# Kernel optimization log

Hardware: AMD Instinct MI355X
Metric: run time of the kernel (lower is better)

Reference implementation:

```python
import jax, jax.numpy as jnp
import numpy as np

# MoE config (matches init_kwargs)
T = 16384   # tokens
H = 1024    # hidden size
I = 1024    # intermediate size per expert
E = 8       # n_experts
TOPK = 2
RENORMALIZE = True


def setup_inputs() -> dict:
    key = jax.random.key(0)
    ks = jax.random.split(key, 6)
    x = jax.random.normal(ks[0], (T, H), dtype=jnp.float32)
    gating_output = jax.random.normal(ks[1], (T, E), dtype=jnp.float32)
    # fp8-quantized weights simulated as their integer-grid values in fp32;
    # dequant = q * per-expert scalar scale (normalize_e4m3fn_to_native_float8 path)
    w1 = jax.random.normal(ks[2], (E, 2 * I, H), dtype=jnp.float32)  # fused [gate; up]
    w2 = jax.random.normal(ks[3], (E, H, I), dtype=jnp.float32)      # down_proj
    w1_scale = jax.random.uniform(ks[4], (E,), dtype=jnp.float32, minval=0.01, maxval=0.05)
    w2_scale = jax.random.uniform(ks[5], (E,), dtype=jnp.float32, minval=0.01, maxval=0.05)
    return {"x": x, "gating_output": gating_output, "w1": w1, "w2": w2,
            "w1_scale": w1_scale, "w2_scale": w2_scale}


def _moe(x, gating_output, w1, w2, w1_scale, w2_scale):
    # softmax scoring -> top-k routing (use_grouped_topk=False)
    probs = jax.nn.softmax(gating_output, axis=-1)              # [T, E]
    topk_w, topk_idx = jax.lax.top_k(probs, TOPK)               # [T, K]
    if RENORMALIZE:
        topk_w = topk_w / jnp.sum(topk_w, axis=-1, keepdims=True)
    out = jnp.zeros_like(x)
    for e in range(E):  # fixed small expert count: grouped-GEMM reference
        w1e = w1[e] * w1_scale[e]                               # dequant [2I, H]
        w2e = w2[e] * w2_scale[e]                               # dequant [H, I]
        gate = x @ w1e[:I].T                                    # [T, I]
        up = x @ w1e[I:].T                                      # [T, I]
        h = jax.nn.silu(gate) * up                              # SwiGLU
        y = h @ w2e.T                                           # [T, H]
        # per-token routing weight for this expert (0 if not routed)
        coef = jnp.sum(jnp.where(topk_idx == e, topk_w, 0.0), axis=-1)  # [T]
        out = out + coef[:, None] * y
    return out


def reference(x, gating_output, w1, w2, w1_scale, w2_scale):
    return _moe(x, gating_output, w1, w2, w1_scale, w2_scale)
```

## Files before the change

### kernel.cpp

```cpp
#include <hip/hip_runtime.h>
#include <hip/hip_bf16.h>

#define T_TOK 16384
#define H_DIM 1024
#define I_DIM 1024
#define E_NUM 8
#define NPAIR (T_TOK * 2)
#define BM 128
#define BK 64
#define MAX_MT (NPAIR / BM + E_NUM)

typedef float v4f __attribute__((ext_vector_type(4)));
typedef float v16f __attribute__((ext_vector_type(16)));
typedef short v8s __attribute__((ext_vector_type(8)));

__device__ __forceinline__ unsigned short f2bf(float f) {
    unsigned int u = __float_as_uint(f);
    unsigned int r = (u + 0x7fffu + ((u >> 16) & 1u)) >> 16;
    return (unsigned short)r;
}
__device__ __forceinline__ float bf2f(unsigned short s) {
    return __uint_as_float(((unsigned int)s) << 16);
}

__device__ __forceinline__ void gl_lds16(const void* g, void* l) {
    __builtin_amdgcn_global_load_lds(
        (const __attribute__((address_space(1))) void*)g,
        (__attribute__((address_space(3))) void*)l, 16, 0, 0);
}

__device__ __forceinline__ int swz(int row, int unit) {
    return row * 64 + ((unit ^ (row & 7)) << 3);
}

__global__ void k_route(const float* __restrict__ gating,
                        int* __restrict__ tokExp, float* __restrict__ tokW,
                        int* __restrict__ counts) {
    int t = blockIdx.x * 256 + threadIdx.x;
    int lane = threadIdx.x & 63;
    float g[E_NUM];
#pragma unroll
    for (int e = 0; e < E_NUM; e++) g[e] = gating[t * E_NUM + e];
    int i0 = 0; float v0 = g[0];
#pragma unroll
    for (int e = 1; e < E_NUM; e++) if (g[e] > v0) { v0 = g[e]; i0 = e; }
    int i1 = -1; float v1 = -1e30f;
#pragma unroll
    for (int e = 0; e < E_NUM; e++) if (e != i0 && g[e] > v1) { v1 = g[e]; i1 = e; }
    float w0 = 1.f / (1.f + __expf(v1 - v0));
    tokExp[2 * t] = i0; tokExp[2 * t + 1] = i1;
    tokW[2 * t] = w0;   tokW[2 * t + 1] = 1.f - w0;
#pragma unroll
    for (int e = 0; e < E_NUM; e++) {
        unsigned long long mA = __ballot(i0 == e);
        unsigned long long mB = __ballot(i1 == e);
        int c = __popcll(mA) + __popcll(mB);
        if (lane == 0 && c) atomicAdd(&counts[e], c);
    }
}

__global__ void k_scan(const int* __restrict__ counts, int* __restrict__ offsets,
                       int* __restrict__ tileOff, int* __restrict__ cursor) {
    if (threadIdx.x == 0 && blockIdx.x == 0) {
        int o = 0, to = 0;
        for (int e = 0; e < E_NUM; e++) {
            offsets[e] = o; tileOff[e] = to; cursor[e] = o;
            o += counts[e];
            to += (counts[e] + BM - 1) / BM;
        }
        offsets[E_NUM] = o; tileOff[E_NUM] = to;
    }
}

__global__ void k_scatter(const int* __restrict__ tokExp, const float* __restrict__ tokW,
                          int* __restrict__ cursor,
                          int* __restrict__ pairTok, float* __restrict__ pairW,
                          int* __restrict__ invMap) {
    int t = blockIdx.x * 256 + threadIdx.x;
    int lane = threadIdx.x & 63;
#pragma unroll
    for (int k = 0; k < 2; k++) {
        int e = tokExp[2 * t + k];
        int pos = 0;
#pragma unroll
        for (int ex = 0; ex < E_NUM; ex++) {
            unsigned long long m = __ballot(e == ex);
            if (m) {
                int leader = __builtin_ctzll(m);
                int base = 0;
                if (lane == leader) base = atomicAdd(&cursor[ex], __popcll(m));
                base = __shfl(base, leader);
                if (e == ex) pos = base + __popcll(m & ((1ull << lane) - 1ull));
            }
        }
        pairTok[pos] = t;
        pairW[pos] = tokW[2 * t + k];
        invMap[2 * t + k] = pos;
    }
}

__global__ void k_cvt_x(const float* __restrict__ src, unsigned short* __restrict__ dst) {
    size_t i4 = ((size_t)blockIdx.x * 256 + threadIdx.x) * 4;
    float4 v = *(const float4*)(src + i4);
    ushort4 o;
    o.x = f2bf(v.x); o.y = f2bf(v.y); o.z = f2bf(v.z); o.w = f2bf(v.w);
    *(ushort4*)(dst + i4) = o;
}

__global__ void k_cvt_w(const float* __restrict__ src, unsigned short* __restrict__ dst,
                        const float* __restrict__ scale, int shift) {
    size_t i4 = ((size_t)blockIdx.x * 256 + threadIdx.x) * 4;
    float s = scale[i4 >> shift];
    float4 v = *(const float4*)(src + i4);
    ushort4 o;
    o.x = f2bf(v.x * s); o.y = f2bf(v.y * s); o.z = f2bf(v.z * s); o.w = f2bf(v.w * s);
    *(ushort4*)(dst + i4) = o;
}

__global__ __launch_bounds__(512, 4)
void k_gemm1(const unsigned short* __restrict__ xbf,
             const unsigned short* __restrict__ w1bf,
             const int* __restrict__ pairTok,
             const int* __restrict__ offsets, const int* __restrict__ tileOff,
             unsigned short* __restrict__ hbuf) {
    __shared__ unsigned short lA[BM * BK];
    __shared__ unsigned short lB[256 * BK];

    int mt = blockIdx.x;
    if (mt >= tileOff[E_NUM]) return;
    int e = 0;
    while (mt >= tileOff[e + 1]) e++;
    int row0 = offsets[e] + (mt - tileOff[e]) * BM;
    int valid = offsets[e + 1] - row0; if (valid > BM) valid = BM;

    int nt = blockIdx.y;
    int tid = threadIdx.x;
    int lane = tid & 63, wave = tid >> 6;
    int role = wave >> 2, quad = wave & 3;
    int wm = quad >> 1, wn = quad & 1;

    int lr = lane >> 3;
    int lcs = ((lane & 7) ^ lr) * 8;

    const unsigned short* wg = w1bf + (size_t)e * 2 * I_DIM * H_DIM + (size_t)(nt * 128) * H_DIM;
    const unsigned short* wu = wg + (size_t)I_DIM * H_DIM;

    int tokRow[2];
#pragma unroll
    for (int j = 0; j < 2; j++) {
        int r = wave * 16 + j * 8 + lr;
        int rc = r < valid ? r : valid - 1;
        tokRow[j] = pairTok[row0 + rc];
    }
    const unsigned short* bRow[4];
#pragma unroll
    for (int j = 0; j < 4; j++) {
        int brow = wave * 32 + j * 8 + lr;
        bRow[j] = (brow < 128) ? (wg + (size_t)brow * H_DIM)
                               : (wu + (size_t)(brow - 128) * H_DIM);
    }

    v16f acc[2][2];
#pragma unroll
    for (int i = 0; i < 2; i++)
#pragma unroll
        for (int j = 0; j < 2; j++) acc[i][j] = (v16f)0.f;

    for (int ko = 0; ko < H_DIM / BK; ko++) {
        int k0 = ko * BK;
        __syncthreads();
#pragma unroll
        for (int j = 0; j < 2; j++)
            gl_lds16(xbf + (size_t)tokRow[j] * H_DIM + k0 + lcs, lA + (wave * 2 + j) * 512);
#pragma unroll
        for (int j = 0; j < 4; j++)
            gl_lds16(bRow[j] + k0 + lcs, lB + (wave * 4 + j) * 512);
        __syncthreads();
#pragma unroll
        for (int kk = 0; kk < BK; kk += 16) {
            int u = (kk >> 3) + (lane >> 5);
            v8s a[2], b[2];
#pragma unroll
            for (int i = 0; i < 2; i++)
                a[i] = *(const v8s*)(lA + swz(wm * 64 + i * 32 + (lane & 31), u));
#pragma unroll
            for (int j = 0; j < 2; j++)
                b[j] = *(const v8s*)(lB + swz(role * 128 + wn * 64 + j * 32 + (lane & 31), u));
#pragma unroll
            for (int i = 0; i < 2; i++)
#pragma unroll
                for (int j = 0; j < 2; j++)
                    acc[i][j] = __builtin_amdgcn_mfma_f32_32x32x16_bf16(a[i], b[j], acc[i][j], 0, 0, 0);
        }
    }

    int half = lane >> 5, c = lane & 31;
    __syncthreads();
    if (role == 1) {
#pragma unroll
        for (int i = 0; i < 2; i++)
#pragma unroll
            for (int r = 0; r < 16; r++) {
                int row = wm * 64 + i * 32 + (r & 3) + 8 * (r >> 2) + 4 * half;
#pragma unroll
                for (int j = 0; j < 2; j++)
                    lB[row * 128 + wn * 64 + j * 32 + c] = f2bf(acc[i][j][r]);
            }
    }
    __syncthreads();
    if (role == 0) {
#pragma unroll
        for (int i = 0; i < 2; i++)
#pragma unroll
            for (int r = 0; r < 16; r++) {
                int row = wm * 64 + i * 32 + (r & 3) + 8 * (r >> 2) + 4 * half;
                if (row < valid) {
                    size_t base = (size_t)(row0 + row) * I_DIM + nt * 128;
#pragma unroll
                    for (int j = 0; j < 2; j++) {
                        float g = acc[i][j][r];
                        float uu = bf2f(lB[row * 128 + wn * 64 + j * 32 + c]);
                        float s = g / (1.f + __expf(-g));
                        hbuf[base + wn * 64 + j * 32 + c] = f2bf(s * uu);
                    }
                }
            }
    }
}

__global__ __launch_bounds__(512, 4)
void k_gemm2(const unsigned short* __restrict__ hbuf,
             const unsigned short* __restrict__ w2bf,
             const float* __restrict__ pairW,
             const int* __restrict__ offsets, const int* __restrict__ tileOff,
             unsigned short* __restrict__ ybuf) {
    __shared__ unsigned short lA[BM * BK];
    __shared__ unsigned short lB[256 * BK];

    int mt = blockIdx.x;
    if (mt >= tileOff[E_NUM]) return;
    int e = 0;
    while (mt >= tileOff[e + 1]) e++;
    int row0 = offsets[e] + (mt - tileOff[e]) * BM;
    int valid = offsets[e + 1] - row0; if (valid > BM) valid = BM;

    int nt = blockIdx.y;
    int tid = threadIdx.x;
    int lane = tid & 63, wave = tid >> 6;
    int wm = wave >> 2, wn = wave & 3;

    int lr = lane >> 3;
    int lcs = ((lane & 7) ^ lr) * 8;

    const unsigned short* w2e = w2bf + (size_t)e * H_DIM * I_DIM + (size_t)(nt * 256) * I_DIM;

    int rowA[2];
#pragma unroll
    for (int j = 0; j < 2; j++) {
        int r = wave * 16 + j * 8 + lr;
        int rc = r < valid ? r : valid - 1;
        rowA[j] = row0 + rc;
    }

    v16f acc[2][2];
#pragma unroll
    for (int i = 0; i < 2; i++)
#pragma unroll
        for (int j = 0; j < 2; j++) acc[i][j] = (v16f)0.f;

    for (int ko = 0; ko < I_DIM / BK; ko++) {
        int k0 = ko * BK;
        __syncthreads();
#pragma unroll
        for (int j = 0; j < 2; j++)
            gl_lds16(hbuf + (size_t)rowA[j] * I_DIM + k0 + lcs, lA + (wave * 2 + j) * 512);
#pragma unroll
        for (int j = 0; j < 4; j++)
            gl_lds16(w2e + (size_t)(wave * 32 + j * 8 + lr) * I_DIM + k0 + lcs,
                     lB + (wave * 4 + j) * 512);
        __syncthreads();
#pragma unroll
        for (int kk = 0; kk < BK; kk += 16) {
            int u = (kk >> 3) + (lane >> 5);
            v8s a[2], b[2];
#pragma unroll
            for (int i = 0; i < 2; i++)
                a[i] = *(const v8s*)(lA + swz(wm * 64 + i * 32 + (lane & 31), u));
#pragma unroll
            for (int j = 0; j < 2; j++)
                b[j] = *(const v8s*)(lB + swz(wn * 64 + j * 32 + (lane & 31), u));
#pragma unroll
            for (int i = 0; i < 2; i++)
#pragma unroll
                for (int j = 0; j < 2; j++)
                    acc[i][j] = __builtin_amdgcn_mfma_f32_32x32x16_bf16(a[i], b[j], acc[i][j], 0, 0, 0);
        }
    }

    int half = lane >> 5, c = lane & 31;
#pragma unroll
    for (int i = 0; i < 2; i++)
#pragma unroll
        for (int r = 0; r < 16; r++) {
            int row = wm * 64 + i * 32 + (r & 3) + 8 * (r >> 2) + 4 * half;
            if (row < valid) {
                int pos = row0 + row;
                float coef = pairW[pos];
                unsigned short* orow = ybuf + (size_t)pos * H_DIM + nt * 256;
#pragma unroll
                for (int j = 0; j < 2; j++)
                    orow[wn * 64 + j * 32 + c] = f2bf(coef * acc[i][j][r]);
            }
        }
}

__global__ __launch_bounds__(256)
void k_reduce(const unsigned short* __restrict__ ybuf,
              const int* __restrict__ invMap,
              float* __restrict__ out) {
    int t = blockIdx.x;
    int p0 = invMap[2 * t], p1 = invMap[2 * t + 1];
    int c4 = threadIdx.x * 4;
    ushort4 a = *(const ushort4*)(ybuf + (size_t)p0 * H_DIM + c4);
    ushort4 b = *(const ushort4*)(ybuf + (size_t)p1 * H_DIM + c4);
    float4 o;
    o.x = bf2f(a.x) + bf2f(b.x);
    o.y = bf2f(a.y) + bf2f(b.y);
    o.z = bf2f(a.z) + bf2f(b.z);
    o.w = bf2f(a.w) + bf2f(b.w);
    *(float4*)(out + (size_t)t * H_DIM + c4) = o;
}

extern "C" void kernel_launch(void* const* d_in, const int* in_sizes, int n_in,
                              void* d_out, int out_size, void* d_ws, size_t ws_size,
                              hipStream_t stream) {
    const float* x      = (const float*)d_in[0];
    const float* gating = (const float*)d_in[1];
    const float* w1     = (const float*)d_in[2];
    const float* w2     = (const float*)d_in[3];
    const float* w1s    = (const float*)d_in[4];
    const float* w2s    = (const float*)d_in[5];
    float* out = (float*)d_out;

    char* ws = (char*)d_ws;
    size_t off = 0;
    auto alloc = [&](size_t bytes) { void* p = ws + off; off += (bytes + 255) & ~(size_t)255; return p; };
    unsigned short* xbf  = (unsigned short*)alloc((size_t)T_TOK * H_DIM * 2);
    unsigned short* w1bf = (unsigned short*)alloc((size_t)E_NUM * 2 * I_DIM * H_DIM * 2);
    unsigned short* w2bf = (unsigned short*)alloc((size_t)E_NUM * H_DIM * I_DIM * 2);
    unsigned short* hbuf = (unsigned short*)alloc((size_t)NPAIR * I_DIM * 2);
    unsigned short* ybuf = (unsigned short*)alloc((size_t)NPAIR * H_DIM * 2);
    int*   pairTok  = (int*)alloc(NPAIR * 4);
    float* pairW    = (float*)alloc(NPAIR * 4);
    int*   tokExp   = (int*)alloc(NPAIR * 4);
    float* tokW     = (float*)alloc(NPAIR * 4);
    int*   invMap   = (int*)alloc(NPAIR * 4);
    int*   counts   = (int*)alloc(64);
    int*   offsets  = (int*)alloc(64);
    int*   tileOff  = (int*)alloc(64);
    int*   cursor   = (int*)alloc(64);

    hipMemsetAsync(counts, 0, 64, stream);

    k_route<<<T_TOK / 256, 256, 0, stream>>>(gating, tokExp, tokW, counts);
    k_scan<<<1, 64, 0, stream>>>(counts, offsets, tileOff, cursor);
    k_scatter<<<T_TOK / 256, 256, 0, stream>>>(tokExp, tokW, cursor, pairTok, pairW, invMap);
    k_cvt_x<<<(T_TOK * H_DIM / 4) / 256, 256, 0, stream>>>(x, xbf);
    k_cvt_w<<<(E_NUM * 2 * I_DIM * H_DIM / 4) / 256, 256, 0, stream>>>(w1, w1bf, w1s, 21);
    k_cvt_w<<<(E_NUM * H_DIM * I_DIM / 4) / 256, 256, 0, stream>>>(w2, w2bf, w2s, 20);

    dim3 g1(MAX_MT, I_DIM / 128);
    k_gemm1<<<g1, 512, 0, stream>>>(xbf, w1bf, pairTok, offsets, tileOff, hbuf);
    dim3 g2(MAX_MT, H_DIM / 256);
    k_gemm2<<<g2, 512, 0, stream>>>(hbuf, w2bf, pairW, offsets, tileOff, ybuf);
    k_reduce<<<T_TOK, 256, 0, stream>>>(ybuf, invMap, out);
}
```

Measured before the change: 561.1 us.

## Use 256x256 tiles with double-buffered LDS and interleaved MFMA/load pipeline

Doubles the M tile to 256 rows so each wave computes a 128x64 sub-tile, which raises arithmetic intensity. Shared memory is double-buffered, and the main loop is split into four phases that interleave LDS reads, async global-to-LDS loads for the stage two iterations ahead, and MFMA bursts under s_setprio and explicit waitcnt. The goal is to hide global load latency and cut the full __syncthreads stalls of the old single-buffer loop. In exchange, occupancy drops to 2 blocks per CU, register pressure is higher, and the larger tiles waste more work on partially filled expert tiles.

Result: slower. 644.7 us (+14.9%).

```diff
diff --git a/kernel.cpp b/kernel.cpp
--- a/kernel.cpp
+++ b/kernel.cpp
@@ -6,8 +6,9 @@
 #define I_DIM 1024
 #define E_NUM 8
 #define NPAIR (T_TOK * 2)
-#define BM 128
+#define BM 256
 #define BK 64
+#define KITER 16
 #define MAX_MT (NPAIR / BM + E_NUM)
 
 typedef float v4f __attribute__((ext_vector_type(4)));
@@ -31,6 +32,37 @@
 
 __device__ __forceinline__ int swz(int row, int unit) {
     return row * 64 + ((unit ^ (row & 7)) << 3);
+}
+
+__device__ __forceinline__ int blkA_of(int w, int j) {
+    int idx = 2 * w + (j & 1);
+    int blk = idx + ((idx >= 8) ? 8 : 0);
+    return blk + ((j >= 2) ? 8 : 0);
+}
+__device__ __forceinline__ int blkB_of(int w, int j) {
+    int idx = 2 * w + (j & 1);
+    int blk = (idx >> 2) * 8 + (idx & 3);
+    return blk + ((j >= 2) ? 4 : 0);
+}
+
+__device__ __forceinline__ void rd_a(const unsigned short* lAc, int rbase, int lane, v8s a[2][4]) {
+#pragma unroll
+    for (int i = 0; i < 2; i++)
+#pragma unroll
+        for (int ks = 0; ks < 4; ks++)
+            a[i][ks] = *(const v8s*)(lAc + swz(rbase + i * 32 + (lane & 31), 2 * ks + (lane >> 5)));
+}
+__device__ __forceinline__ void rd_b(const unsigned short* lBc, int rbase, int lane, v8s b[4]) {
+#pragma unroll
+    for (int ks = 0; ks < 4; ks++)
+        b[ks] = *(const v8s*)(lBc + swz(rbase + (lane & 31), 2 * ks + (lane >> 5)));
+}
+__device__ __forceinline__ void mfma8(const v8s a[2][4], const v8s b[4], v16f* c0, v16f* c1) {
+#pragma unroll
+    for (int ks = 0; ks < 4; ks++) {
+        *c0 = __builtin_amdgcn_mfma_f32_32x32x16_bf16(a[0][ks], b[ks], *c0, 0, 0, 0);
+        *c1 = __builtin_amdgcn_mfma_f32_32x32x16_bf16(a[1][ks], b[ks], *c1, 0, 0, 0);
+    }
 }
 
 __global__ void k_route(const float* __restrict__ gating,
@@ -117,14 +149,65 @@
     *(ushort4*)(dst + i4) = o;
 }
 
-__global__ __launch_bounds__(512, 4)
+#define STG_A(buf, j, k0) gl_lds16(aSrc[j] + (k0) + lcs, &lA[buf][aoff[j]])
+#define STG_B(buf, j, k0) gl_lds16(bSrc[j] + (k0) + lcs, &lB[buf][boff[j]])
+
+#define GEMM_MAINLOOP                                                          \
+    for (int T = 0; T < KITER; T++) {                                          \
+        int cur = T & 1;                                                       \
+        const unsigned short* lAc = lA[cur];                                   \
+        const unsigned short* lBc = lB[cur];                                   \
+        int k2 = (T + 2) * BK;                                                 \
+        bool s2 = (T + 2 < KITER);                                             \
+                                            \
+        rd_a(lAc, wm * 128, lane, a);                                          \
+        rd_b(lBc, bbase, lane, b0);                                            \
+        __builtin_amdgcn_s_barrier();                                          \
+        __builtin_amdgcn_s_setprio(1);                                         \
+        mfma8(a, b0, &acc[0][0], &acc[1][0]);                                  \
+        __builtin_amdgcn_s_setprio(0);                                         \
+        __builtin_amdgcn_s_barrier();                                          \
+                                     \
+        rd_b(lBc, bbase + 32, lane, b1);                                       \
+        if (s2) { STG_B(cur, 0, k2); STG_B(cur, 1, k2); }                      \
+        __builtin_amdgcn_s_barrier();                                          \
+        __builtin_amdgcn_s_setprio(1);                                         \
+        mfma8(a, b1, &acc[0][1], &acc[1][1]);                                  \
+        __builtin_amdgcn_s_setprio(0);                                         \
+        __builtin_amdgcn_s_barrier();                                          \
+                                   \
+        rd_a(lAc, wm * 128 + 64, lane, a);                                     \
+        if (s2) { STG_B(cur, 2, k2); STG_B(cur, 3, k2); }                      \
+        __builtin_amdgcn_s_barrier();                                          \
+        __builtin_amdgcn_s_setprio(1);                                         \
+        mfma8(a, b0, &acc[2][0], &acc[3][0]);                                  \
+        __builtin_amdgcn_s_setprio(0);                                         \
+        __builtin_amdgcn_s_barrier();                                          \
+                          \
+        if (s2) {                                                              \
+            STG_A(cur, 0, k2); STG_A(cur, 1, k2);                              \
+            STG_A(cur, 2, k2); STG_A(cur, 3, k2);                              \
+            asm volatile("s_waitcnt vmcnt(8)" ::: "memory");                    \
+        } else if (T + 1 < KITER) {                                            \
+            asm volatile("s_waitcnt vmcnt(0)" ::: "memory");                    \
+        }                                                                      \
+        __builtin_amdgcn_sched_barrier(0);                                     \
+        __builtin_amdgcn_s_barrier();                                          \
+        __builtin_amdgcn_s_setprio(1);                                         \
+        mfma8(a, b1, &acc[2][1], &acc[3][1]);                                  \
+        __builtin_amdgcn_s_setprio(0);                                         \
+        __builtin_amdgcn_s_barrier();                                          \
+        __builtin_amdgcn_sched_barrier(0);                                     \
+    }
+
+__global__ __launch_bounds__(512, 2)
 void k_gemm1(const unsigned short* __restrict__ xbf,
              const unsigned short* __restrict__ w1bf,
              const int* __restrict__ pairTok,
              const int* __restrict__ offsets, const int* __restrict__ tileOff,
              unsigned short* __restrict__ hbuf) {
-    __shared__ unsigned short lA[BM * BK];
-    __shared__ unsigned short lB[256 * BK];
+    __shared__ unsigned short lA[2][BM * BK];
+    __shared__ unsigned short lB[2][BM * BK];
 
     int mt = blockIdx.x;
     if (mt >= tileOff[E_NUM]) return;
@@ -136,90 +219,75 @@
     int nt = blockIdx.y;
     int tid = threadIdx.x;
     int lane = tid & 63, wave = tid >> 6;
-    int role = wave >> 2, quad = wave & 3;
-    int wm = quad >> 1, wn = quad & 1;
-
+    int wm = wave >> 2, wn = wave & 3;
     int lr = lane >> 3;
     int lcs = ((lane & 7) ^ lr) * 8;
+    int bbase = (wn & 1) * 64 + (wn >> 1) * 128;
 
     const unsigned short* wg = w1bf + (size_t)e * 2 * I_DIM * H_DIM + (size_t)(nt * 128) * H_DIM;
     const unsigned short* wu = wg + (size_t)I_DIM * H_DIM;
 
-    int tokRow[2];
-#pragma unroll
-    for (int j = 0; j < 2; j++) {
-        int r = wave * 16 + j * 8 + lr;
-        int rc = r < valid ? r : valid - 1;
-        tokRow[j] = pairTok[row0 + rc];
-    }
-    const unsigned short* bRow[4];
+    const unsigned short* aSrc[4];
+    const unsigned short* bSrc[4];
+    int aoff[4], boff[4];
 #pragma unroll
     for (int j = 0; j < 4; j++) {
-        int brow = wave * 32 + j * 8 + lr;
-        bRow[j] = (brow < 128) ? (wg + (size_t)brow * H_DIM)
-                               : (wu + (size_t)(brow - 128) * H_DIM);
-    }
-
-    v16f acc[2][2];
-#pragma unroll
-    for (int i = 0; i < 2; i++)
-#pragma unroll
-        for (int j = 0; j < 2; j++) acc[i][j] = (v16f)0.f;
-
-    for (int ko = 0; ko < H_DIM / BK; ko++) {
-        int k0 = ko * BK;
-        __syncthreads();
-#pragma unroll
-        for (int j = 0; j < 2; j++)
-            gl_lds16(xbf + (size_t)tokRow[j] * H_DIM + k0 + lcs, lA + (wave * 2 + j) * 512);
-#pragma unroll
-        for (int j = 0; j < 4; j++)
-            gl_lds16(bRow[j] + k0 + lcs, lB + (wave * 4 + j) * 512);
-        __syncthreads();
-#pragma unroll
-        for (int kk = 0; kk < BK; kk += 16) {
-            int u = (kk >> 3) + (lane >> 5);
-            v8s a[2], b[2];
-#pragma unroll
-            for (int i = 0; i < 2; i++)
-                a[i] = *(const v8s*)(lA + swz(wm * 64 + i * 32 + (lane & 31), u));
-#pragma unroll
-            for (int j = 0; j < 2; j++)
-                b[j] = *(const v8s*)(lB + swz(role * 128 + wn * 64 + j * 32 + (lane & 31), u));
-#pragma unroll
-            for (int i = 0; i < 2; i++)
+        int ab = blkA_of(wave, j), bb = blkB_of(wave, j);
+        aoff[j] = ab * 512; boff[j] = bb * 512;
+        int ra = ab * 8 + lr;
+        int rc = ra < valid ? ra : valid - 1;
+        aSrc[j] = xbf + (size_t)pairTok[row0 + rc] * H_DIM;
+        int rb = bb * 8 + lr;
+        bSrc[j] = (rb < 128) ? (wg + (size_t)rb * H_DIM) : (wu + (size_t)(rb - 128) * H_DIM);
+    }
+
+    v16f acc[4][2];
+#pragma unroll
+    for (int i = 0; i < 4; i++) { acc[i][0] = (v16f)0.f; acc[i][1] = (v16f)0.f; }
+
+#pragma unroll
+    for (int j = 0; j < 4; j++) STG_A(0, j, 0);
+#pragma unroll
+    for (int j = 0; j < 4; j++) STG_B(0, j, 0);
+#pragma unroll
+    for (int j = 0; j < 4; j++) STG_B(1, j, BK);
+#pragma unroll
+    for (int j = 0; j < 4; j++) STG_A(1, j, BK);
+    asm volatile("s_waitcnt vmcnt(8)" ::: "memory");
+    __builtin_amdgcn_sched_barrier(0);
+    __builtin_amdgcn_s_barrier();
+
+    v8s a[2][4], b0[4], b1[4];
+#pragma unroll 2
+    GEMM_MAINLOOP
+
+    __syncthreads();
+    unsigned short* uLds = &lA[0][0];
+    int half = lane >> 5, c = lane & 31;
+    if (wn >= 2) {
+#pragma unroll
+        for (int i = 0; i < 4; i++)
+#pragma unroll
+            for (int r = 0; r < 16; r++) {
+                int row = wm * 128 + i * 32 + (r & 3) + 8 * (r >> 2) + 4 * half;
 #pragma unroll
                 for (int j = 0; j < 2; j++)
-                    acc[i][j] = __builtin_amdgcn_mfma_f32_32x32x16_bf16(a[i], b[j], acc[i][j], 0, 0, 0);
-        }
-    }
-
-    int half = lane >> 5, c = lane & 31;
+                    uLds[row * 128 + (wn - 2) * 64 + j * 32 + c] = f2bf(acc[i][j][r]);
+            }
+    }
     __syncthreads();
-    if (role == 1) {
-#pragma unroll
-        for (int i = 0; i < 2; i++)
+    if (wn < 2) {
+#pragma unroll
+        for (int i = 0; i < 4; i++)
 #pragma unroll
             for (int r = 0; r < 16; r++) {
-                int row = wm * 64 + i * 32 + (r & 3) + 8 * (r >> 2) + 4 * half;
-#pragma unroll
-                for (int j = 0; j < 2; j++)
-                    lB[row * 128 + wn * 64 + j * 32 + c] = f2bf(acc[i][j][r]);
-            }
-    }
-    __syncthreads();
-    if (role == 0) {
-#pragma unroll
-        for (int i = 0; i < 2; i++)
-#pragma unroll
-            for (int r = 0; r < 16; r++) {
-                int row = wm * 64 + i * 32 + (r & 3) + 8 * (r >> 2) + 4 * half;
+                int row = wm * 128 + i * 32 + (r & 3) + 8 * (r >> 2) + 4 * half;
                 if (row < valid) {
                     size_t base = (size_t)(row0 + row) * I_DIM + nt * 128;
 #pragma unroll
                     for (int j = 0; j < 2; j++) {
                         float g = acc[i][j][r];
-                        float uu = bf2f(lB[row * 128 + wn * 64 + j * 32 + c]);
+                        float uu = bf2f(uLds[row * 128 + wn * 64 + j * 32 + c]);
                         float s = g / (1.f + __expf(-g));
                         hbuf[base + wn * 64 + j * 32 + c] = f2bf(s * uu);
                     }
@@ -228,14 +296,14 @@
     }
 }
 
-__global__ __launch_bounds__(512, 4)
+__global__ __launch_bounds__(512, 2)
 void k_gemm2(const unsigned short* __restrict__ hbuf,
              const unsigned short* __restrict__ w2bf,
              const float* __restrict__ pairW,
              const int* __restrict__ offsets, const int* __restrict__ tileOff,
              unsigned short* __restrict__ ybuf) {
-    __shared__ unsigned short lA[BM * BK];
-    __shared__ unsigned short lB[256 * BK];
+    __shared__ unsigned short lA[2][BM * BK];
+    __shared__ unsigned short lB[2][BM * BK];
 
     int mt = blockIdx.x;
     if (mt >= tileOff[E_NUM]) return;
@@ -248,68 +316,58 @@
     int tid = threadIdx.x;
     int lane = tid & 63, wave = tid >> 6;
     int wm = wave >> 2, wn = wave & 3;
-
     int lr = lane >> 3;
     int lcs = ((lane & 7) ^ lr) * 8;
+    int bbase = wn * 64;
 
     const unsigned short* w2e = w2bf + (size_t)e * H_DIM * I_DIM + (size_t)(nt * 256) * I_DIM;
 
-    int rowA[2];
-#pragma unroll
-    for (int j = 0; j < 2; j++) {
-        int r = wave * 16 + j * 8 + lr;
-        int rc = r < valid ? r : valid - 1;
-        rowA[j] = row0 + rc;
-    }
-
-    v16f acc[2][2];
-#pragma unroll
-    for (int i = 0; i < 2; i++)
-#pragma unroll
-        for (int j = 0; j < 2; j++) acc[i][j] = (v16f)0.f;
-
-    for (int ko = 0; ko < I_DIM / BK; ko++) {
-        int k0 = ko * BK;
-        __syncthreads();
-#pragma unroll
-        for (int j = 0; j < 2; j++)
-            gl_lds16(hbuf + (size_t)rowA[j] * I_DIM + k0 + lcs, lA + (wave * 2 + j) * 512);
-#pragma unroll
-        for (int j = 0; j < 4; j++)
-            gl_lds16(w2e + (size_t)(wave * 32 + j * 8 + lr) * I_DIM + k0 + lcs,
-                     lB + (wave * 4 + j) * 512);
-        __syncthreads();
-#pragma unroll
-        for (int kk = 0; kk < BK; kk += 16) {
-            int u = (kk >> 3) + (lane >> 5);
-            v8s a[2], b[2];
-#pragma unroll
-            for (int i = 0; i < 2; i++)
-                a[i] = *(const v8s*)(lA + swz(wm * 64 + i * 32 + (lane & 31), u));
-#pragma unroll
-            for (int j = 0; j < 2; j++)
-                b[j] = *(const v8s*)(lB + swz(wn * 64 + j * 32 + (lane & 31), u));
-#pragma unroll
-            for (int i = 0; i < 2; i++)
-#pragma unroll
-                for (int j = 0; j < 2; j++)
-                    acc[i][j] = __builtin_amdgcn_mfma_f32_32x32x16_bf16(a[i], b[j], acc[i][j], 0, 0, 0);
-        }
-    }
+    const unsigned short* aSrc[4];
+    const unsigned short* bSrc[4];
+    int aoff[4], boff[4];
+#pragma unroll
+    for (int j = 0; j < 4; j++) {
+        int ab = blkA_of(wave, j), bb = blkB_of(wave, j);
+        aoff[j] = ab * 512; boff[j] = bb * 512;
+        int ra = ab * 8 + lr;
+        int rc = ra < valid ? ra : valid - 1;
+        aSrc[j] = hbuf + (size_t)(row0 + rc) * I_DIM;
+        bSrc[j] = w2e + (size_t)(bb * 8 + lr) * I_DIM;
+    }
+
+    v16f acc[4][2];
+#pragma unroll
+    for (int i = 0; i < 4; i++) { acc[i][0] = (v16f)0.f; acc[i][1] = (v16f)0.f; }
+
+#pragma unroll
+    for (int j = 0; j < 4; j++) STG_A(0, j, 0);
+#pragma unroll
+    for (int j = 0; j < 4; j++) STG_B(0, j, 0);
+#pragma unroll
+    for (int j = 0; j < 4; j++) STG_B(1, j, BK);
+#pragma unroll
+    for (int j = 0; j < 4; j++) STG_A(1, j, BK);
+    asm volatile("s_waitcnt vmcnt(8)" ::: "memory");
+    __builtin_amdgcn_sched_barrier(0);
+    __builtin_amdgcn_s_barrier();
+
+    v8s a[2][4], b0[4], b1[4];
+#pragma unroll 2
+    GEMM_MAINLOOP
 
     int half = lane >> 5, c = lane & 31;
 #pragma unroll
-    for (int i = 0; i < 2; i++)
+    for (int i = 0; i < 4; i++)
 #pragma unroll
         for (int r = 0; r < 16; r++) {
-            int row = wm * 64 + i * 32 + (r & 3) + 8 * (r >> 2) + 4 * half;
+            int row = wm * 128 + i * 32 + (r & 3) + 8 * (r >> 2) + 4 * half;
             if (row < valid) {
                 int pos = row0 + row;
                 float coef = pairW[pos];
                 unsigned short* orow = ybuf + (size_t)pos * H_DIM + nt * 256;
 #pragma unroll
                 for (int j = 0; j < 2; j++)
-                    orow[wn * 64 + j * 32 + c] = f2bf(coef * acc[i][j][r]);
+                    orow[bbase + j * 32 + c] = f2bf(coef * acc[i][j][r]);
             }
         }
 }
```

## Fuse expert combine into GEMM2 via atomics, merge conversion kernels, swizzle LDS

Applied to the files above, without the earlier changes.

GEMM2 now scales each row by its routing weight and atomically adds it into the fp32 output at the token row, which removes the bf16 intermediate buffer and the separate reduce kernel. The output is zeroed with a memset first. The three conversion kernels are merged into one launch. The gemm1 epilogue LDS staging uses an XOR swizzle to cut bank conflicts. Atomics add contention and make the summation order nondeterministic, and the memset adds a full output write.

Measured after the change: 650.3 us. +15.9%, slower.

```diff
diff --git a/kernel.cpp b/kernel.cpp
--- a/kernel.cpp
+++ b/kernel.cpp
@@ -74,8 +74,7 @@
 
 __global__ void k_scatter(const int* __restrict__ tokExp, const float* __restrict__ tokW,
                           int* __restrict__ cursor,
-                          int* __restrict__ pairTok, float* __restrict__ pairW,
-                          int* __restrict__ invMap) {
+                          int* __restrict__ pairTok, float* __restrict__ pairW) {
     int t = blockIdx.x * 256 + threadIdx.x;
     int lane = threadIdx.x & 63;
 #pragma unroll
@@ -95,26 +94,26 @@
         }
         pairTok[pos] = t;
         pairW[pos] = tokW[2 * t + k];
-        invMap[2 * t + k] = pos;
-    }
-}
-
-__global__ void k_cvt_x(const float* __restrict__ src, unsigned short* __restrict__ dst) {
+    }
+}
+
+__global__ void k_cvt_all(const float* __restrict__ x,
+                          const float* __restrict__ w1, const float* __restrict__ w2,
+                          const float* __restrict__ w1s, const float* __restrict__ w2s,
+                          unsigned short* __restrict__ xbf,
+                          unsigned short* __restrict__ w1bf,
+                          unsigned short* __restrict__ w2bf) {
+    const size_t N0 = (size_t)T_TOK * H_DIM;
+    const size_t N1 = (size_t)E_NUM * 2 * I_DIM * H_DIM;
     size_t i4 = ((size_t)blockIdx.x * 256 + threadIdx.x) * 4;
-    float4 v = *(const float4*)(src + i4);
-    ushort4 o;
-    o.x = f2bf(v.x); o.y = f2bf(v.y); o.z = f2bf(v.z); o.w = f2bf(v.w);
-    *(ushort4*)(dst + i4) = o;
-}
-
-__global__ void k_cvt_w(const float* __restrict__ src, unsigned short* __restrict__ dst,
-                        const float* __restrict__ scale, int shift) {
-    size_t i4 = ((size_t)blockIdx.x * 256 + threadIdx.x) * 4;
-    float s = scale[i4 >> shift];
-    float4 v = *(const float4*)(src + i4);
+    const float* src; unsigned short* dst; size_t off; float s;
+    if (i4 < N0)            { src = x;  dst = xbf;  off = i4;           s = 1.f; }
+    else if (i4 < N0 + N1)  { src = w1; dst = w1bf; off = i4 - N0;      s = w1s[off >> 21]; }
+    else                    { src = w2; dst = w2bf; off = i4 - N0 - N1; s = w2s[off >> 20]; }
+    float4 v = *(const float4*)(src + off);
     ushort4 o;
     o.x = f2bf(v.x * s); o.y = f2bf(v.y * s); o.z = f2bf(v.z * s); o.w = f2bf(v.w * s);
-    *(ushort4*)(dst + i4) = o;
+    *(ushort4*)(dst + off) = o;
 }
 
 __global__ __launch_bounds__(512, 4)
@@ -203,8 +202,10 @@
             for (int r = 0; r < 16; r++) {
                 int row = wm * 64 + i * 32 + (r & 3) + 8 * (r >> 2) + 4 * half;
 #pragma unroll
-                for (int j = 0; j < 2; j++)
-                    lB[row * 128 + wn * 64 + j * 32 + c] = f2bf(acc[i][j][r]);
+                for (int j = 0; j < 2; j++) {
+                    int cs = (j * 32 + c) ^ ((row & 4) << 3);
+                    lB[row * 128 + wn * 64 + cs] = f2bf(acc[i][j][r]);
+                }
             }
     }
     __syncthreads();
@@ -219,7 +220,8 @@
 #pragma unroll
                     for (int j = 0; j < 2; j++) {
                         float g = acc[i][j][r];
-                        float uu = bf2f(lB[row * 128 + wn * 64 + j * 32 + c]);
+                        int cs = (j * 32 + c) ^ ((row & 4) << 3);
+                        float uu = bf2f(lB[row * 128 + wn * 64 + cs]);
                         float s = g / (1.f + __expf(-g));
                         hbuf[base + wn * 64 + j * 32 + c] = f2bf(s * uu);
                     }
@@ -231,9 +233,9 @@
 __global__ __launch_bounds__(512, 4)
 void k_gemm2(const unsigned short* __restrict__ hbuf,
              const unsigned short* __restrict__ w2bf,
-             const float* __restrict__ pairW,
+             const float* __restrict__ pairW, const int* __restrict__ pairTok,
              const int* __restrict__ offsets, const int* __restrict__ tileOff,
-             unsigned short* __restrict__ ybuf) {
+             float* __restrict__ out) {
     __shared__ unsigned short lA[BM * BK];
     __shared__ unsigned short lB[256 * BK];
 
@@ -306,29 +308,13 @@
             if (row < valid) {
                 int pos = row0 + row;
                 float coef = pairW[pos];
-                unsigned short* orow = ybuf + (size_t)pos * H_DIM + nt * 256;
+                int tok = pairTok[pos];
+                float* orow = out + (size_t)tok * H_DIM + nt * 256;
 #pragma unroll
                 for (int j = 0; j < 2; j++)
-                    orow[wn * 64 + j * 32 + c] = f2bf(coef * acc[i][j][r]);
+                    atomicAdd(&orow[wn * 64 + j * 32 + c], coef * acc[i][j][r]);
             }
         }
-}
-
-__global__ __launch_bounds__(256)
-void k_reduce(const unsigned short* __restrict__ ybuf,
-              const int* __restrict__ invMap,
-              float* __restrict__ out) {
-    int t = blockIdx.x;
-    int p0 = invMap[2 * t], p1 = invMap[2 * t + 1];
-    int c4 = threadIdx.x * 4;
-    ushort4 a = *(const ushort4*)(ybuf + (size_t)p0 * H_DIM + c4);
-    ushort4 b = *(const ushort4*)(ybuf + (size_t)p1 * H_DIM + c4);
-    float4 o;
-    o.x = bf2f(a.x) + bf2f(b.x);
-    o.y = bf2f(a.y) + bf2f(b.y);
-    o.z = bf2f(a.z) + bf2f(b.z);
-    o.w = bf2f(a.w) + bf2f(b.w);
-    *(float4*)(out + (size_t)t * H_DIM + c4) = o;
 }
 
 extern "C" void kernel_launch(void* const* d_in, const int* in_sizes, int n_in,
@@ -349,29 +335,28 @@
     unsigned short* w1bf = (unsigned short*)alloc((size_t)E_NUM * 2 * I_DIM * H_DIM * 2);
     unsigned short* w2bf = (unsigned short*)alloc((size_t)E_NUM * H_DIM * I_DIM * 2);
     unsigned short* hbuf = (unsigned short*)alloc((size_t)NPAIR * I_DIM * 2);
-    unsigned short* ybuf = (unsigned short*)alloc((size_t)NPAIR * H_DIM * 2);
     int*   pairTok  = (int*)alloc(NPAIR * 4);
     float* pairW    = (float*)alloc(NPAIR * 4);
     int*   tokExp   = (int*)alloc(NPAIR * 4);
     float* tokW     = (float*)alloc(NPAIR * 4);
-    int*   invMap   = (int*)alloc(NPAIR * 4);
     int*   counts   = (int*)alloc(64);
     int*   offsets  = (int*)alloc(64);
     int*   tileOff  = (int*)alloc(64);
     int*   cursor   = (int*)alloc(64);
 
     hipMemsetAsync(counts, 0, 64, stream);
+    hipMemsetAsync(out, 0, (size_t)T_TOK * H_DIM * 4, stream);
 
     k_route<<<T_TOK / 256, 256, 0, stream>>>(gating, tokExp, tokW, counts);
     k_scan<<<1, 64, 0, stream>>>(counts, offsets, tileOff, cursor);
-    k_scatter<<<T_TOK / 256, 256, 0, stream>>>(tokExp, tokW, cursor, pairTok, pairW, invMap);
-    k_cvt_x<<<(T_TOK * H_DIM / 4) / 256, 256, 0, stream>>>(x, xbf);
-    k_cvt_w<<<(E_NUM * 2 * I_DIM * H_DIM / 4) / 256, 256, 0, stream>>>(w1, w1bf, w1s, 21);
-    k_cvt_w<<<(E_NUM * H_DIM * I_DIM / 4) / 256, 256, 0, stream>>>(w2, w2bf, w2s, 20);
+    k_scatter<<<T_TOK / 256, 256, 0, stream>>>(tokExp, tokW, cursor, pairTok, pairW);
+
+    size_t ncvt = ((size_t)T_TOK * H_DIM + (size_t)E_NUM * 2 * I_DIM * H_DIM +
+                   (size_t)E_NUM * H_DIM * I_DIM) / 4 / 256;
+    k_cvt_all<<<(int)ncvt, 256, 0, stream>>>(x, w1, w2, w1s, w2s, xbf, w1bf, w2bf);
 
     dim3 g1(MAX_MT, I_DIM / 128);
     k_gemm1<<<g1, 512, 0, stream>>>(xbf, w1bf, pairTok, offsets, tileOff, hbuf);
     dim3 g2(MAX_MT, H_DIM / 256);
-    k_gemm2<<<g2, 512, 0, stream>>>(hbuf, w2bf, pairW, offsets, tileOff, ybuf);
-    k_reduce<<<T_TOK, 256, 0, stream>>>(ybuf, invMap, out);
-}
+    k_gemm2<<<g2, 512, 0, stream>>>(hbuf, w2bf, pairW, pairTok, offsets, tileOff, out);
+}
```
